# Kernel tuning notes

Hardware: AMD Instinct MI355X
Metric: run time of the kernel (lower is better)

## Reference

```python
import jax, jax.numpy as jnp
import numpy as np

LATENT_CH = 64  # feature_ch // 8


def conv1x1(x, w):
    # Conv2dLayer with kernel_size=1, bias=False, activation='linear':
    # weight_gain = 1/sqrt(in_channels * 1)
    gain = 1.0 / np.sqrt(w.shape[1])
    return jnp.einsum('bchw,oc->bohw', x, w * gain)


def casual_attention(q, k, v):
    # q,k,v: [B, C, N] / [B, C, M]; score = q^T k, softmax over keys, out = score @ v^T
    score = jnp.einsum('bcn,bcm->bnm', q, k)
    score = jax.nn.softmax(score, axis=-1)
    return jnp.einsum('bnm,bcm->bnc', score, v)  # [B, N, C]


def reference(feature_map, concepts, w_theta, w_phi, w_g, w_o, gamma_sa, gamma_moca):
    B, C, H, W = feature_map.shape
    L = LATENT_CH
    HW = H * W

    # ---- SelfAttention ----
    th = conv1x1(feature_map, w_theta).reshape(B, L, HW)
    ph = conv1x1(feature_map, w_phi).reshape(B, L, HW)
    g = conv1x1(feature_map, w_g).reshape(B, L, HW)
    # torch does .view(-1, L, H, W) on a [B, HW, L] tensor -> raw memory reinterpret
    lat = casual_attention(th, ph, g).reshape(B, L, H, W)
    sa_out = gamma_sa * conv1x1(lat, w_o) + feature_map

    # ---- MomentumConceptAttention (theta and o shared with SA, trainable_conv=False) ----
    enc = conv1x1(sa_out, w_theta).reshape(B, L, HW)
    phi_c = concepts.T[None]                      # [1, L, P]  (torch.no_grad on concepts)
    phi_c = jnp.broadcast_to(phi_c, (B, L, concepts.shape[0]))
    lat2 = casual_attention(enc, phi_c, phi_c).reshape(B, L, H, W)
    out = gamma_moca * conv1x1(lat2, w_o) + sa_out
    return out


def setup_inputs() -> dict:
    key = jax.random.key(0)
    ks = jax.random.split(key, 8)
    B, C, H, W = 8, 512, 64, 64
    L, P = LATENT_CH, 256
    return {
        'feature_map': jax.random.normal(ks[0], (B, C, H, W), jnp.float32),
        'concepts': jax.random.normal(ks[1], (P, L), jnp.float32),
        'w_theta': jax.random.normal(ks[2], (L, C), jnp.float32),
        'w_phi': jax.random.normal(ks[3], (L, C), jnp.float32),
        'w_g': jax.random.normal(ks[4], (L, C), jnp.float32),
        'w_o': jax.random.normal(ks[5], (C, L), jnp.float32),
        'gamma_sa': jnp.float32(0.1),
        'gamma_moca': jnp.float32(0.1),
    }
```

## Files before the change

kernel.cpp:

```cpp
#include <hip/hip_runtime.h>
#include <math.h>

#define HW   4096
#define CINP 512
#define LCH  64

typedef short bf8 __attribute__((ext_vector_type(8)));
typedef float f4  __attribute__((ext_vector_type(4)));

__device__ __forceinline__ unsigned short f2bf(float x) {
    union { float f; unsigned int u; } v; v.f = x;
    return (unsigned short)((v.u + 0x7fffu + ((v.u >> 16) & 1u)) >> 16);
}
__device__ __forceinline__ bf8 ldbf8(const unsigned short* p) {
    uint4 u = *(const uint4*)p;
    return __builtin_bit_cast(bf8, u);
}
__device__ __forceinline__ unsigned int cvtpk(float a, float b) {
    unsigned int r;
    asm volatile("v_cvt_pk_bf16_f32 %0, %1, %2" : "=v"(r) : "v"(a), "v"(b));
    return r;
}

__global__ __launch_bounds__(256) void precast(
    const float* __restrict__ wt, const float* __restrict__ wp,
    const float* __restrict__ wg, const float* __restrict__ wo,
    const float* __restrict__ conc,
    unsigned short* __restrict__ WB, unsigned short* __restrict__ WO,
    unsigned short* __restrict__ CK, unsigned short* __restrict__ CV)
{
    const float gain = 0.04419417382415922f;
    int id = blockIdx.x * 256 + threadIdx.x;
    if (id < 98304) {
        int o = id >> 9, k = id & 511;
        const float* w = (o < 64) ? wt : (o < 128) ? wp : wg;
        WB[id] = f2bf(w[(o & 63) * 512 + k] * gain);
    } else if (id < 131072) {
        int j = id - 98304;
        WO[j] = f2bf(wo[j]);
    } else if (id < 147456) {
        int j = id - 131072;
        CK[j] = f2bf(conc[j]);
    } else if (id < 163840) {
        int j = id - 147456;
        int l = j >> 8, m = j & 255;
        CV[j] = f2bf(conc[m * 64 + l]);
    }
}

__global__ __launch_bounds__(256) void cast_transpose(const float* __restrict__ x,
                                                      unsigned short* __restrict__ XT)
{
    __shared__ unsigned short Lb[64][72];
    const int t  = threadIdx.x;
    const int n0 = blockIdx.x * 64, c0 = blockIdx.y * 64, b = blockIdx.z;
    const float* xb = x + ((size_t)b * CINP + c0) * HW + n0;
    const int cc = t >> 4, n4 = (t & 15) * 4;
    #pragma unroll
    for (int i = 0; i < 4; i++) {
        int c = cc + i * 16;
        float4 v = *(const float4*)(xb + (size_t)c * HW + n4);
        Lb[n4 + 0][c] = f2bf(v.x);
        Lb[n4 + 1][c] = f2bf(v.y);
        Lb[n4 + 2][c] = f2bf(v.z);
        Lb[n4 + 3][c] = f2bf(v.w);
    }
    __syncthreads();
    const int n = t & 63, cb0 = t >> 6;
    unsigned short* orow = XT + ((size_t)b * HW + n0 + n) * CINP + c0;
    #pragma unroll
    for (int i = 0; i < 2; i++) {
        int cb = cb0 + i * 4;
        *(uint4*)(orow + cb * 8) = *(const uint4*)&Lb[n][cb * 8];
    }
}

__global__ __launch_bounds__(256) void lat_transpose(const unsigned short* __restrict__ A,
                                                     unsigned short* __restrict__ LT)
{
    __shared__ unsigned short Ls[64][72];
    const int t = threadIdx.x, s0 = blockIdx.x * 64, b = blockIdx.y;
    const unsigned short* ab = A + (size_t)b * LCH * HW;
    #pragma unroll
    for (int it = 0; it < 2; it++) {
        int c = (t >> 3) + it * 32, s8 = (t & 7) * 8;
        union { uint4 u; unsigned short s[8]; } v;
        v.u = *(const uint4*)(ab + (size_t)c * HW + s0 + s8);
        #pragma unroll
        for (int i = 0; i < 8; i++) Ls[s8 + i][c] = v.s[i];
    }
    __syncthreads();
    unsigned short* ob = LT + ((size_t)b * HW + s0) * LCH;
    #pragma unroll
    for (int it = 0; it < 2; it++) {
        int s = (t >> 3) + it * 32, c8 = (t & 7);
        *(uint4*)(ob + (size_t)s * LCH + c8 * 8) = *(const uint4*)&Ls[s][c8 * 8];
    }
}

template <int NRT>
__global__ __launch_bounds__(256) void qkv_gemm(unsigned short* XT,
                                                const unsigned short* __restrict__ WB,
                                                unsigned short* __restrict__ VL)
{
    const int t = threadIdx.x;
    const int wave = t >> 6, lane = t & 63, quad = lane >> 4, lidx = lane & 15;
    const int b = blockIdx.y;
    const int ncol = blockIdx.x * 64 + wave * 16 + lidx;
    unsigned short* xrow = XT + ((size_t)b * HW + ncol) * CINP;

    f4 acc[NRT];
    #pragma unroll
    for (int r = 0; r < NRT; r++) acc[r] = (f4){0.f, 0.f, 0.f, 0.f};

    for (int kk = 0; kk < 16; kk++) {
        const int k0 = kk * 32 + quad * 8;
        bf8 bq = ldbf8(xrow + k0);
        #pragma unroll
        for (int rt = 0; rt < NRT; rt++) {
            bf8 aw = ldbf8(WB + (size_t)(rt * 16 + lidx) * CINP + k0);
            acc[rt] = __builtin_amdgcn_mfma_f32_16x16x32_bf16(aw, bq, acc[rt], 0, 0, 0);
        }
    }

    #pragma unroll
    for (int rt = 0; rt < NRT; rt++) {
        if (rt < 8) {
            union { unsigned short s[4]; uint2 u; } pk;
            #pragma unroll
            for (int r = 0; r < 4; r++) pk.s[r] = f2bf(acc[rt][r]);
            int off = (rt < 4) ? (rt * 16 + quad * 4) : (64 + (rt - 4) * 16 + quad * 4);
            *(uint2*)(xrow + off) = pk.u;
        } else {
            #pragma unroll
            for (int r = 0; r < 4; r++) {
                int l = (rt - 8) * 16 + quad * 4 + r;
                VL[((size_t)b * LCH + l) * HW + ncol] = f2bf(acc[rt][r]);
            }
        }
    }
}

__global__ __launch_bounds__(256) void flash(
    const unsigned short* Qb, size_t qbat,
    const unsigned short* Kb, size_t krow, size_t kbat,
    const unsigned short* Vb, size_t vrow, size_t vbat,
    unsigned short* __restrict__ Aout, int nkeys)
{
    __shared__ __align__(16) unsigned short Ks[2][32][72];
    __shared__ __align__(16) unsigned short Vs[2][64][40];
    __shared__ __align__(16) unsigned short Ps[4][32][40];

    const int t = threadIdx.x;
    const int wave = t >> 6, lane = t & 63, quad = lane >> 4, lidx = lane & 15;
    const int b = blockIdx.y, q0 = blockIdx.x * 128 + wave * 32;

    const unsigned short* qp = Qb + (size_t)b * qbat;
    const unsigned short* kp = Kb + (size_t)b * kbat;
    const unsigned short* vp = Vb + (size_t)b * vbat;

    const int krt = t >> 3, kch = (t & 7) * 8;
    const int vrt = t >> 2, vch = (t & 3) * 8;

    bf8 qa[2][2];
    #pragma unroll
    for (int qb = 0; qb < 2; qb++)
        #pragma unroll
        for (int kh = 0; kh < 2; kh++)
            qa[qb][kh] = ldbf8(qp + (size_t)(q0 + qb * 16 + lidx) * CINP + kh * 32 + quad * 8);

    f4 O[2][4];
    float Lp[2] = {0.f, 0.f};
    #pragma unroll
    for (int qb = 0; qb < 2; qb++)
        #pragma unroll
        for (int lt = 0; lt < 4; lt++) O[qb][lt] = (f4){0.f, 0.f, 0.f, 0.f};

    const int nt = nkeys >> 5;

    {
        uint4 k0v = *(const uint4*)(kp + (size_t)krt * krow + kch);
        uint4 v0v = *(const uint4*)(vp + (size_t)vrt * vrow + vch);
        *(uint4*)&Ks[0][krt][kch] = k0v;
        *(uint4*)&Vs[0][vrt][vch] = v0v;
    }
    __syncthreads();

    for (int tl = 0; tl < nt; tl++) {
        const int cur = tl & 1;
        const bool pf = (tl + 1 < nt);
        uint4 kpre, vpre;
        if (pf) {
            const int m1 = (tl + 1) * 32;
            kpre = *(const uint4*)(kp + (size_t)(m1 + krt) * krow + kch);
            vpre = *(const uint4*)(vp + (size_t)vrt * vrow + m1 + vch);
        }

        bf8 kf[2][2];
        #pragma unroll
        for (int ms = 0; ms < 2; ms++)
            #pragma unroll
            for (int kh = 0; kh < 2; kh++)
                kf[ms][kh] = *(const bf8*)&Ks[cur][ms * 16 + lidx][kh * 32 + quad * 8];

        f4 S[2][2];
        #pragma unroll
        for (int qb = 0; qb < 2; qb++)
            #pragma unroll
            for (int ms = 0; ms < 2; ms++) {
                f4 s = (f4){0.f, 0.f, 0.f, 0.f};
                s = __builtin_amdgcn_mfma_f32_16x16x32_bf16(kf[ms][0], qa[qb][0], s, 0, 0, 0);
                s = __builtin_amdgcn_mfma_f32_16x16x32_bf16(kf[ms][1], qa[qb][1], s, 0, 0, 0);
                S[qb][ms] = s;
            }

        #pragma unroll
        for (int qb = 0; qb < 2; qb++)
            #pragma unroll
            for (int ms = 0; ms < 2; ms++) {
                float p0 = __expf(S[qb][ms][0]);
                float p1 = __expf(S[qb][ms][1]);
                float p2 = __expf(S[qb][ms][2]);
                float p3 = __expf(S[qb][ms][3]);
                Lp[qb] += (p0 + p1) + (p2 + p3);
                uint2 pk;
                pk.x = cvtpk(p0, p1);
                pk.y = cvtpk(p2, p3);
                *(uint2*)&Ps[wave][qb * 16 + lidx][ms * 16 + quad * 4] = pk;
            }

        bf8 pf0 = *(const bf8*)&Ps[wave][lidx][quad * 8];
        bf8 pf1 = *(const bf8*)&Ps[wave][16 + lidx][quad * 8];
        #pragma unroll
        for (int lt = 0; lt < 4; lt++) {
            bf8 vf = *(const bf8*)&Vs[cur][lt * 16 + lidx][quad * 8];
            O[0][lt] = __builtin_amdgcn_mfma_f32_16x16x32_bf16(pf0, vf, O[0][lt], 0, 0, 0);
            O[1][lt] = __builtin_amdgcn_mfma_f32_16x16x32_bf16(pf1, vf, O[1][lt], 0, 0, 0);
        }

        if (pf) {
            *(uint4*)&Ks[cur ^ 1][krt][kch] = kpre;
            *(uint4*)&Vs[cur ^ 1][vrt][vch] = vpre;
        }
        __syncthreads();
    }

    float inv[2];
    #pragma unroll
    for (int qb = 0; qb < 2; qb++) {
        float s = Lp[qb];
        s += __shfl_xor(s, 16);
        s += __shfl_xor(s, 32);
        inv[qb] = 1.f / s;
    }
    #pragma unroll
    for (int qb = 0; qb < 2; qb++)
        #pragma unroll
        for (int r = 0; r < 4; r++) {
            float iv = __shfl(inv[qb], quad * 4 + r);
            size_t n = (size_t)b * HW + q0 + qb * 16 + quad * 4 + r;
            #pragma unroll
            for (int lt = 0; lt < 4; lt++)
                Aout[n * LCH + lt * 16 + lidx] = f2bf(O[qb][lt][r] * iv);
        }
}

__global__ __launch_bounds__(256) void conv_o(const unsigned short* __restrict__ LT,
                                              const unsigned short* __restrict__ WO,
                                              const float* __restrict__ res,
                                              const float* __restrict__ gamma_p,
                                              float* __restrict__ out,
                                              unsigned short* ST)
{
    const int t = threadIdx.x;
    const int wave = t >> 6, lane = t & 63, quad = lane >> 4, lidx = lane & 15;
    const int b = blockIdx.z, o0 = blockIdx.y * 64;
    const int scol = blockIdx.x * 64 + wave * 16 + lidx;
    const unsigned short* arow = LT + ((size_t)b * HW + scol) * LCH;

    f4 acc[4];
    #pragma unroll
    for (int ot = 0; ot < 4; ot++) acc[ot] = (f4){0.f, 0.f, 0.f, 0.f};

    #pragma unroll
    for (int kh = 0; kh < 2; kh++) {
        bf8 bq = ldbf8(arow + kh * 32 + quad * 8);
        #pragma unroll
        for (int ot = 0; ot < 4; ot++) {
            bf8 af = ldbf8(WO + (size_t)(o0 + ot * 16 + lidx) * LCH + kh * 32 + quad * 8);
            acc[ot] = __builtin_amdgcn_mfma_f32_16x16x32_bf16(af, bq, acc[ot], 0, 0, 0);
        }
    }

    const float scale = gamma_p[0] * 0.125f;
    #pragma unroll
    for (int ot = 0; ot < 4; ot++) {
        float v[4];
        #pragma unroll
        for (int r = 0; r < 4; r++) {
            size_t idx = ((size_t)b * CINP + o0 + ot * 16 + quad * 4 + r) * HW + scol;
            v[r] = fmaf(scale, acc[ot][r], res[idx]);
            out[idx] = v[r];
        }
        if (ST) {
            union { unsigned short s[4]; uint2 u; } pk;
            #pragma unroll
            for (int r = 0; r < 4; r++) pk.s[r] = f2bf(v[r]);
            *(uint2*)(ST + ((size_t)b * HW + scol) * CINP + o0 + ot * 16 + quad * 4) = pk.u;
        }
    }
}

extern "C" void kernel_launch(void* const* d_in, const int* in_sizes, int n_in,
                              void* d_out, int out_size, void* d_ws, size_t ws_size,
                              hipStream_t stream)
{
    const float* f    = (const float*)d_in[0];
    const float* conc = (const float*)d_in[1];
    const float* wt   = (const float*)d_in[2];
    const float* wp   = (const float*)d_in[3];
    const float* wg   = (const float*)d_in[4];
    const float* wo   = (const float*)d_in[5];
    const float* gsa  = (const float*)d_in[6];
    const float* gmo  = (const float*)d_in[7];
    float* out = (float*)d_out;

    char* ws = (char*)d_ws;
    unsigned short* XT = (unsigned short*)ws;
    unsigned short* VL = (unsigned short*)(ws + ((size_t)32 << 20));
    unsigned short* LT = VL;
    unsigned short* A1 = (unsigned short*)(ws + ((size_t)36 << 20));
    unsigned short* WB = (unsigned short*)(ws + ((size_t)40 << 20));
    unsigned short* WO = WB + 192 * 512;
    unsigned short* CK = WO + 512 * 64;
    unsigned short* CV = CK + 256 * 64;

    dim3 blk256(256);

    precast<<<640, blk256, 0, stream>>>(wt, wp, wg, wo, conc, WB, WO, CK, CV);
    cast_transpose<<<dim3(64, 8, 8), blk256, 0, stream>>>(f, XT);

    qkv_gemm<12><<<dim3(64, 8), blk256, 0, stream>>>(XT, WB, VL);
    flash<<<dim3(32, 8), blk256, 0, stream>>>(
        XT, (size_t)HW * CINP,
        XT + 64, CINP, (size_t)HW * CINP,
        VL, HW, (size_t)LCH * HW,
        A1, HW);
    lat_transpose<<<dim3(64, 8), blk256, 0, stream>>>(A1, LT);
    conv_o<<<dim3(64, 8, 8), blk256, 0, stream>>>(LT, WO, f, gsa, out, XT );

    qkv_gemm<4><<<dim3(64, 8), blk256, 0, stream>>>(XT , WB , nullptr);
    flash<<<dim3(32, 8), blk256, 0, stream>>>(
        XT, (size_t)HW * CINP,
        CK, LCH, 0,
        CV, 256, 0,
        A1 , 256);
    lat_transpose<<<dim3(64, 8), blk256, 0, stream>>>(A1, LT);
    conv_o<<<dim3(64, 8, 8), blk256, 0, stream>>>(LT, WO, out, gmo, out, nullptr);
}
```

Baseline: 397.2 us.

## Shrink flash blocks to two waves and pass P via permlane swaps

The flash attention kernel now runs 128-thread blocks covering 64 queries, which doubles the grid from 256 to 512 blocks. Each thread loads two K and two V vectors per tile to keep the staging the same size. The exponentiated scores are rearranged into MFMA A-operand layout in registers using permlane32/permlane16 swaps, which removes the per-wave LDS scratch buffer and its write/read round trip. The goal is better CU occupancy on a small grid and less LDS traffic, at the cost of more load instructions per thread and reliance on gfx950-specific permlane intrinsics.

Measured after the change: 399.9 us. Within noise of the previous version (+0.7%).

```diff
diff --git a/kernel.cpp b/kernel.cpp
--- a/kernel.cpp
+++ b/kernel.cpp
@@ -7,6 +7,7 @@
 
 typedef short bf8 __attribute__((ext_vector_type(8)));
 typedef float f4  __attribute__((ext_vector_type(4)));
+typedef unsigned int u32x2 __attribute__((ext_vector_type(2)));
 
 __device__ __forceinline__ unsigned short f2bf(float x) {
     union { float f; unsigned int u; } v; v.f = x;
@@ -141,7 +142,7 @@
     }
 }
 
-__global__ __launch_bounds__(256) void flash(
+__global__ __launch_bounds__(128) void flash(
     const unsigned short* Qb, size_t qbat,
     const unsigned short* Kb, size_t krow, size_t kbat,
     const unsigned short* Vb, size_t vrow, size_t vbat,
@@ -149,18 +150,19 @@
 {
     __shared__ __align__(16) unsigned short Ks[2][32][72];
     __shared__ __align__(16) unsigned short Vs[2][64][40];
-    __shared__ __align__(16) unsigned short Ps[4][32][40];
 
     const int t = threadIdx.x;
     const int wave = t >> 6, lane = t & 63, quad = lane >> 4, lidx = lane & 15;
-    const int b = blockIdx.y, q0 = blockIdx.x * 128 + wave * 32;
+    const int b = blockIdx.y, q0 = blockIdx.x * 64 + wave * 32;
 
     const unsigned short* qp = Qb + (size_t)b * qbat;
     const unsigned short* kp = Kb + (size_t)b * kbat;
     const unsigned short* vp = Vb + (size_t)b * vbat;
 
-    const int krt = t >> 3, kch = (t & 7) * 8;
-    const int vrt = t >> 2, vch = (t & 3) * 8;
+    const int kkey0 = t >> 3, kch = t & 7;
+    const int kkey1 = kkey0 + 16;
+    const int vr0 = t >> 2, vch = t & 3;
+    const int vr1 = vr0 + 32;
 
     bf8 qa[2][2];
     #pragma unroll
@@ -179,21 +181,27 @@
     const int nt = nkeys >> 5;
 
     {
-        uint4 k0v = *(const uint4*)(kp + (size_t)krt * krow + kch);
-        uint4 v0v = *(const uint4*)(vp + (size_t)vrt * vrow + vch);
-        *(uint4*)&Ks[0][krt][kch] = k0v;
-        *(uint4*)&Vs[0][vrt][vch] = v0v;
+        uint4 k0 = *(const uint4*)(kp + (size_t)kkey0 * krow + kch * 8);
+        uint4 k1 = *(const uint4*)(kp + (size_t)kkey1 * krow + kch * 8);
+        uint4 v0 = *(const uint4*)(vp + (size_t)vr0 * vrow + vch * 8);
+        uint4 v1 = *(const uint4*)(vp + (size_t)vr1 * vrow + vch * 8);
+        *(uint4*)&Ks[0][kkey0][kch * 8] = k0;
+        *(uint4*)&Ks[0][kkey1][kch * 8] = k1;
+        *(uint4*)&Vs[0][vr0][vch * 8] = v0;
+        *(uint4*)&Vs[0][vr1][vch * 8] = v1;
     }
     __syncthreads();
 
     for (int tl = 0; tl < nt; tl++) {
         const int cur = tl & 1;
-        const bool pf = (tl + 1 < nt);
-        uint4 kpre, vpre;
-        if (pf) {
+        const bool pfv = (tl + 1 < nt);
+        uint4 kq0, kq1, vq0, vq1;
+        if (pfv) {
             const int m1 = (tl + 1) * 32;
-            kpre = *(const uint4*)(kp + (size_t)(m1 + krt) * krow + kch);
-            vpre = *(const uint4*)(vp + (size_t)vrt * vrow + m1 + vch);
+            kq0 = *(const uint4*)(kp + (size_t)(m1 + kkey0) * krow + kch * 8);
+            kq1 = *(const uint4*)(kp + (size_t)(m1 + kkey1) * krow + kch * 8);
+            vq0 = *(const uint4*)(vp + (size_t)vr0 * vrow + m1 + vch * 8);
+            vq1 = *(const uint4*)(vp + (size_t)vr1 * vrow + m1 + vch * 8);
         }
 
         bf8 kf[2][2];
@@ -214,33 +222,36 @@
                 S[qb][ms] = s;
             }
 
-        #pragma unroll
-        for (int qb = 0; qb < 2; qb++)
-            #pragma unroll
-            for (int ms = 0; ms < 2; ms++) {
-                float p0 = __expf(S[qb][ms][0]);
-                float p1 = __expf(S[qb][ms][1]);
-                float p2 = __expf(S[qb][ms][2]);
-                float p3 = __expf(S[qb][ms][3]);
-                Lp[qb] += (p0 + p1) + (p2 + p3);
-                uint2 pk;
-                pk.x = cvtpk(p0, p1);
-                pk.y = cvtpk(p2, p3);
-                *(uint2*)&Ps[wave][qb * 16 + lidx][ms * 16 + quad * 4] = pk;
-            }
-
-        bf8 pf0 = *(const bf8*)&Ps[wave][lidx][quad * 8];
-        bf8 pf1 = *(const bf8*)&Ps[wave][16 + lidx][quad * 8];
+        bf8 pa[2];
+        #pragma unroll
+        for (int qb = 0; qb < 2; qb++) {
+            float e00 = __expf(S[qb][0][0]), e01 = __expf(S[qb][0][1]);
+            float e02 = __expf(S[qb][0][2]), e03 = __expf(S[qb][0][3]);
+            float e10 = __expf(S[qb][1][0]), e11 = __expf(S[qb][1][1]);
+            float e12 = __expf(S[qb][1][2]), e13 = __expf(S[qb][1][3]);
+            Lp[qb] += ((e00 + e01) + (e02 + e03)) + ((e10 + e11) + (e12 + e13));
+            unsigned int A = cvtpk(e00, e01), B = cvtpk(e02, e03);
+            unsigned int C = cvtpk(e10, e11), D = cvtpk(e12, e13);
+            u32x2 ac = __builtin_amdgcn_permlane32_swap(A, C, false, false);
+            u32x2 xz = __builtin_amdgcn_permlane16_swap(ac.x, ac.y, false, false);
+            u32x2 bd = __builtin_amdgcn_permlane32_swap(B, D, false, false);
+            u32x2 yw = __builtin_amdgcn_permlane16_swap(bd.x, bd.y, false, false);
+            uint4 pu; pu.x = xz.x; pu.y = yw.x; pu.z = xz.y; pu.w = yw.y;
+            pa[qb] = __builtin_bit_cast(bf8, pu);
+        }
+
         #pragma unroll
         for (int lt = 0; lt < 4; lt++) {
             bf8 vf = *(const bf8*)&Vs[cur][lt * 16 + lidx][quad * 8];
-            O[0][lt] = __builtin_amdgcn_mfma_f32_16x16x32_bf16(pf0, vf, O[0][lt], 0, 0, 0);
-            O[1][lt] = __builtin_amdgcn_mfma_f32_16x16x32_bf16(pf1, vf, O[1][lt], 0, 0, 0);
-        }
-
-        if (pf) {
-            *(uint4*)&Ks[cur ^ 1][krt][kch] = kpre;
-            *(uint4*)&Vs[cur ^ 1][vrt][vch] = vpre;
+            O[0][lt] = __builtin_amdgcn_mfma_f32_16x16x32_bf16(pa[0], vf, O[0][lt], 0, 0, 0);
+            O[1][lt] = __builtin_amdgcn_mfma_f32_16x16x32_bf16(pa[1], vf, O[1][lt], 0, 0, 0);
+        }
+
+        if (pfv) {
+            *(uint4*)&Ks[cur ^ 1][kkey0][kch * 8] = kq0;
+            *(uint4*)&Ks[cur ^ 1][kkey1][kch * 8] = kq1;
+            *(uint4*)&Vs[cur ^ 1][vr0][vch * 8] = vq0;
+            *(uint4*)&Vs[cur ^ 1][vr1][vch * 8] = vq1;
         }
         __syncthreads();
     }
@@ -335,13 +346,13 @@
     unsigned short* CK = WO + 512 * 64;
     unsigned short* CV = CK + 256 * 64;
 
-    dim3 blk256(256);
+    dim3 blk256(256), blk128(128);
 
     precast<<<640, blk256, 0, stream>>>(wt, wp, wg, wo, conc, WB, WO, CK, CV);
     cast_transpose<<<dim3(64, 8, 8), blk256, 0, stream>>>(f, XT);
 
     qkv_gemm<12><<<dim3(64, 8), blk256, 0, stream>>>(XT, WB, VL);
-    flash<<<dim3(32, 8), blk256, 0, stream>>>(
+    flash<<<dim3(64, 8), blk128, 0, stream>>>(
         XT, (size_t)HW * CINP,
         XT + 64, CINP, (size_t)HW * CINP,
         VL, HW, (size_t)LCH * HW,
@@ -350,7 +361,7 @@
     conv_o<<<dim3(64, 8, 8), blk256, 0, stream>>>(LT, WO, f, gsa, out, XT );
 
     qkv_gemm<4><<<dim3(64, 8), blk256, 0, stream>>>(XT , WB , nullptr);
-    flash<<<dim3(32, 8), blk256, 0, stream>>>(
+    flash<<<dim3(64, 8), blk128, 0, stream>>>(
         XT, (size_t)HW * CINP,
         CK, LCH, 0,
         CV, 256, 0,
```
